# Optimization experiments

Measured on AMD Instinct MI355X. Metric: run time of the kernel, lower is better.

## Reference

```python
import jax, jax.numpy as jnp
import numpy as np

N = 8192
D = 128
LMBD = 0.1
SPARSITY = 0.99  # fraction of zero entries in A


def setup_inputs() -> dict:
    key = jax.random.key(0)
    kA, kW = jax.random.split(key)
    u = jax.random.uniform(kA, (N, N), dtype=jnp.float32)
    A = jnp.where(u > SPARSITY, u, 0.0)
    W = jax.random.normal(kW, (N, D), dtype=jnp.float32) * 0.02
    b = jnp.zeros((D,), dtype=jnp.float32)
    return {"A": A, "W": W, "b": b}


def reference(A, W, b):
    # model(tf.eye(N)) with Dense(d) == eye(N) @ W + b == W + b  -> [N, d]
    Y = W + b
    # main loss: 0.5 * sum(mask * (A - Y Y^T)^2), mask = (A > 0)
    R = A - jnp.matmul(Y, Y.T)  # [N, N]
    main_loss = 0.5 * jnp.sum(jnp.where(A > 0, R * R, 0.0))
    # reg loss: lmbd/2 * ||Y||_F^2
    reg_loss = 0.5 * LMBD * jnp.sum(Y * Y)
    return main_loss + reg_loss
```

## Files before the change

kernel.cpp:

```cpp
#include <hip/hip_runtime.h>

#define N 8192
#define D 128
#define MAXNZ 256

__device__ __forceinline__ float wave_reduce(float p) {
    #pragma unroll
    for (int off = 32; off > 0; off >>= 1)
        p += __shfl_xor(p, off, 64);
    return p;
}

__global__ __launch_bounds__(256, 8)
void gf_main_kernel(const float* __restrict__ A,
                    const float* __restrict__ W,
                    const float* __restrict__ b,
                    float* __restrict__ partials) {
    __shared__ int   s_col[4][MAXNZ];
    __shared__ float s_val[4][MAXNZ];
    __shared__ float s_bsum[4];

    const int lane = threadIdx.x & 63;
    const int w    = threadIdx.x >> 6;
    const int row  = blockIdx.x * 4 + w;

    const float2 bb = ((const float2*)b)[lane];
    float2 yi = ((const float2*)(W + (size_t)row * D))[lane];
    yi.x += bb.x; yi.y += bb.y;

    const float4* Arow = (const float4*)(A + (size_t)row * N);
    const unsigned long long ltmask = (lane == 63) ? ~0ull >> 1 : (1ull << lane) - 1ull;
    int cnt = 0;
    for (int it = 0; it < N / 256; ++it) {
        const float4 a4 = Arow[it * 64 + lane];
        const float av[4] = {a4.x, a4.y, a4.z, a4.w};
        #pragma unroll
        for (int q = 0; q < 4; ++q) {
            const unsigned long long m = __ballot(av[q] > 0.0f);
            if (av[q] > 0.0f) {
                const int pos = cnt + __popcll(m & ((1ull << lane) - 1ull));
                if (pos < MAXNZ) {
                    s_col[w][pos] = it * 256 + lane * 4 + q;
                    s_val[w][pos] = av[q];
                }
            }
            cnt += __popcll(m);
        }
    }
    if (cnt > MAXNZ) cnt = MAXNZ;
    __syncthreads();

    float acc = 0.0f;
    for (int t = 0; t < cnt; t += 4) {
        float p[4];
        float av[4];
        #pragma unroll
        for (int k = 0; k < 4; ++k) {
            const bool valid = (t + k) < cnt;
            const int  idx   = valid ? (t + k) : 0;
            const int  j     = s_col[w][idx];
            av[k]            = valid ? s_val[w][idx] : 0.0f;
            const float2 yj  = ((const float2*)(W + (size_t)j * D))[lane];
            p[k] = yi.x * (yj.x + bb.x) + yi.y * (yj.y + bb.y);
        }
        #pragma unroll
        for (int off = 32; off > 0; off >>= 1) {
            #pragma unroll
            for (int k = 0; k < 4; ++k)
                p[k] += __shfl_xor(p[k], off, 64);
        }
        #pragma unroll
        for (int k = 0; k < 4; ++k) {
            if ((t + k) < cnt) {
                const float r = av[k] - p[k];
                acc += r * r;
            }
        }
    }

    const float reg = wave_reduce(yi.x * yi.x + yi.y * yi.y);
    const float total = 0.5f * acc + 0.05f * reg;
    if (lane == 0) s_bsum[w] = total;
    __syncthreads();
    if (threadIdx.x == 0)
        partials[blockIdx.x] = s_bsum[0] + s_bsum[1] + s_bsum[2] + s_bsum[3];
}

__global__ __launch_bounds__(256)
void gf_reduce_kernel(const float* __restrict__ partials, float* __restrict__ out) {
    __shared__ float s_ws[4];
    const int lane = threadIdx.x & 63;
    const int w    = threadIdx.x >> 6;
    float s = 0.0f;
    for (int i = threadIdx.x; i < N / 4; i += 256) s += partials[i];
    s = wave_reduce(s);
    if (lane == 0) s_ws[w] = s;
    __syncthreads();
    if (threadIdx.x == 0) out[0] = s_ws[0] + s_ws[1] + s_ws[2] + s_ws[3];
}

extern "C" void kernel_launch(void* const* d_in, const int* in_sizes, int n_in,
                              void* d_out, int out_size, void* d_ws, size_t ws_size,
                              hipStream_t stream) {
    const float* A = (const float*)d_in[0];
    const float* W = (const float*)d_in[1];
    const float* b = (const float*)d_in[2];
    float* out = (float*)d_out;
    float* partials = (float*)d_ws;

    gf_main_kernel<<<dim3(N / 4), dim3(256), 0, stream>>>(A, W, b, partials);
    gf_reduce_kernel<<<dim3(1), dim3(256), 0, stream>>>(partials, out);
}
```

Measured before the change: 413.4 us.

## Software-pipeline A row loads and W gathers with register prefetch

The scan over each A row now keeps four float4 loads per lane in flight and prefetches the next 1024-column chunk while ballot-compacting the current one. The gather loop over nonzeros also prefetches the next group of four W rows before reducing the current group. Occupancy bounds drop from 8 to 6 blocks per CU to make room for the extra prefetch registers. The goal is more memory-level parallelism on the 256 MB A stream, at the cost of fewer resident waves.

After: 391.4 us. 1.06x faster.

```diff
diff --git a/kernel.cpp b/kernel.cpp
--- a/kernel.cpp
+++ b/kernel.cpp
@@ -11,7 +11,7 @@
     return p;
 }
 
-__global__ __launch_bounds__(256, 8)
+__global__ __launch_bounds__(256, 6)
 void gf_main_kernel(const float* __restrict__ A,
                     const float* __restrict__ W,
                     const float* __restrict__ b,
@@ -29,46 +29,84 @@
     yi.x += bb.x; yi.y += bb.y;
 
     const float4* Arow = (const float4*)(A + (size_t)row * N);
-    const unsigned long long ltmask = (lane == 63) ? ~0ull >> 1 : (1ull << lane) - 1ull;
+    const unsigned long long lmask = (1ull << lane) - 1ull;
+
+    float4 pf[4];
+    #pragma unroll
+    for (int k = 0; k < 4; ++k) pf[k] = Arow[k * 64 + lane];
+
     int cnt = 0;
-    for (int it = 0; it < N / 256; ++it) {
-        const float4 a4 = Arow[it * 64 + lane];
-        const float av[4] = {a4.x, a4.y, a4.z, a4.w};
+    for (int it = 0; it < 8; ++it) {
+        float4 cur[4];
         #pragma unroll
-        for (int q = 0; q < 4; ++q) {
-            const unsigned long long m = __ballot(av[q] > 0.0f);
-            if (av[q] > 0.0f) {
-                const int pos = cnt + __popcll(m & ((1ull << lane) - 1ull));
-                if (pos < MAXNZ) {
-                    s_col[w][pos] = it * 256 + lane * 4 + q;
-                    s_val[w][pos] = av[q];
+        for (int k = 0; k < 4; ++k) cur[k] = pf[k];
+        if (it < 7) {
+            #pragma unroll
+            for (int k = 0; k < 4; ++k)
+                pf[k] = Arow[(it + 1) * 256 + k * 64 + lane];
+        }
+        #pragma unroll
+        for (int k = 0; k < 4; ++k) {
+            const int base_col = (it * 4 + k) * 256 + lane * 4;
+            const float av4[4] = {cur[k].x, cur[k].y, cur[k].z, cur[k].w};
+            #pragma unroll
+            for (int q = 0; q < 4; ++q) {
+                const unsigned long long m = __ballot(av4[q] > 0.0f);
+                if (av4[q] > 0.0f) {
+                    const int pos = cnt + __popcll(m & lmask);
+                    if (pos < MAXNZ) {
+                        s_col[w][pos] = base_col + q;
+                        s_val[w][pos] = av4[q];
+                    }
                 }
+                cnt += __popcll(m);
             }
-            cnt += __popcll(m);
         }
     }
     if (cnt > MAXNZ) cnt = MAXNZ;
     __syncthreads();
 
     float acc = 0.0f;
+    float2 yjn[4];
+    float  avn[4];
+    #pragma unroll
+    for (int k = 0; k < 4; ++k) {
+        const bool valid = k < cnt;
+        const int  idx   = valid ? k : 0;
+        const int  j     = s_col[w][idx];
+        avn[k]           = valid ? s_val[w][idx] : 0.0f;
+        yjn[k]           = ((const float2*)(W + (size_t)j * D))[lane];
+    }
+
     for (int t = 0; t < cnt; t += 4) {
+        float2 yj[4];
+        float  av[4];
+        #pragma unroll
+        for (int k = 0; k < 4; ++k) { yj[k] = yjn[k]; av[k] = avn[k]; }
+
+        if (t + 4 < cnt) {
+            #pragma unroll
+            for (int k = 0; k < 4; ++k) {
+                const bool valid = (t + 4 + k) < cnt;
+                const int  idx   = valid ? (t + 4 + k) : 0;
+                const int  j     = s_col[w][idx];
+                avn[k]           = valid ? s_val[w][idx] : 0.0f;
+                yjn[k]           = ((const float2*)(W + (size_t)j * D))[lane];
+            }
+        }
+
         float p[4];
-        float av[4];
         #pragma unroll
-        for (int k = 0; k < 4; ++k) {
-            const bool valid = (t + k) < cnt;
-            const int  idx   = valid ? (t + k) : 0;
-            const int  j     = s_col[w][idx];
-            av[k]            = valid ? s_val[w][idx] : 0.0f;
-            const float2 yj  = ((const float2*)(W + (size_t)j * D))[lane];
-            p[k] = yi.x * (yj.x + bb.x) + yi.y * (yj.y + bb.y);
-        }
+        for (int k = 0; k < 4; ++k)
+            p[k] = yi.x * (yj[k].x + bb.x) + yi.y * (yj[k].y + bb.y);
+
         #pragma unroll
         for (int off = 32; off > 0; off >>= 1) {
             #pragma unroll
             for (int k = 0; k < 4; ++k)
                 p[k] += __shfl_xor(p[k], off, 64);
         }
+
         #pragma unroll
         for (int k = 0; k < 4; ++k) {
             if ((t + k) < cnt) {
```

## Replace sparse gather with dense fp16 MFMA tiled Y·Yᵀ and masked loss

Applied to the files above, without the earlier changes.

Replaces the per-row nonzero compaction and gather of Y rows with a dense 128x128-tile computation of Y·Yᵀ using fp16 MFMA 16x16x32 instructions. A prep kernel first converts Y=W+b to fp16 and computes the regularization term. The tile kernel then streams A once and accumulates masked squared residuals. This removes the ballot/compaction and the scattered row gathers but does full dense N²·D work. The fp16 inputs may lose precision relative to the fp32 reference.

Result: faster. 383.7 us (-7.2%).

```diff
diff --git a/kernel.cpp b/kernel.cpp
--- a/kernel.cpp
+++ b/kernel.cpp
@@ -1,8 +1,15 @@
 #include <hip/hip_runtime.h>
+#include <hip/hip_fp16.h>
 
 #define N 8192
 #define D 128
-#define MAXNZ 256
+
+typedef _Float16 f16x8 __attribute__((ext_vector_type(8)));
+typedef float    f32x4 __attribute__((ext_vector_type(4)));
+
+#define YH_OFF    0
+#define PART_OFF  (4u * 1024 * 1024)
+#define NPART     (4096 + 2048)
 
 __device__ __forceinline__ float wave_reduce(float p) {
     #pragma unroll
@@ -11,79 +18,94 @@
     return p;
 }
 
-__global__ __launch_bounds__(256, 8)
-void gf_main_kernel(const float* __restrict__ A,
-                    const float* __restrict__ W,
-                    const float* __restrict__ b,
-                    float* __restrict__ partials) {
-    __shared__ int   s_col[4][MAXNZ];
-    __shared__ float s_val[4][MAXNZ];
+__global__ __launch_bounds__(256)
+void gf_prep_kernel(const float* __restrict__ W, const float* __restrict__ b,
+                    __half* __restrict__ Yh, float* __restrict__ partials) {
     __shared__ float s_bsum[4];
-
     const int lane = threadIdx.x & 63;
     const int w    = threadIdx.x >> 6;
     const int row  = blockIdx.x * 4 + w;
 
     const float2 bb = ((const float2*)b)[lane];
-    float2 yi = ((const float2*)(W + (size_t)row * D))[lane];
-    yi.x += bb.x; yi.y += bb.y;
+    float2 y = ((const float2*)(W + (size_t)row * D))[lane];
+    y.x += bb.x; y.y += bb.y;
+    __half2 h;
+    h.x = __float2half_rn(y.x);
+    h.y = __float2half_rn(y.y);
+    ((__half2*)(Yh + (size_t)row * D))[lane] = h;
 
-    const float4* Arow = (const float4*)(A + (size_t)row * N);
-    const unsigned long long ltmask = (lane == 63) ? ~0ull >> 1 : (1ull << lane) - 1ull;
-    int cnt = 0;
-    for (int it = 0; it < N / 256; ++it) {
-        const float4 a4 = Arow[it * 64 + lane];
-        const float av[4] = {a4.x, a4.y, a4.z, a4.w};
+    const float reg = wave_reduce(y.x * y.x + y.y * y.y);
+    if (lane == 0) s_bsum[w] = reg;
+    __syncthreads();
+    if (threadIdx.x == 0)
+        partials[4096 + blockIdx.x] = 0.05f * (s_bsum[0] + s_bsum[1] + s_bsum[2] + s_bsum[3]);
+}
+
+__global__ __launch_bounds__(256)
+void gf_tile_kernel(const float* __restrict__ A,
+                    const __half* __restrict__ Yh,
+                    float* __restrict__ partials) {
+    __shared__ float s_bsum[4];
+    const int lane = threadIdx.x & 63;
+    const int w    = threadIdx.x >> 6;
+    const int tx   = blockIdx.x & 63;
+    const int ty   = blockIdx.x >> 6;
+    const int i0   = ty * 128 + (w >> 1) * 64;
+    const int j0   = tx * 128 + (w & 1) * 64;
+    const int lr   = lane & 15;
+    const int kg   = lane >> 4;
+
+    f32x4 acc[4][4];
+    #pragma unroll
+    for (int bi = 0; bi < 4; ++bi)
         #pragma unroll
-        for (int q = 0; q < 4; ++q) {
-            const unsigned long long m = __ballot(av[q] > 0.0f);
-            if (av[q] > 0.0f) {
-                const int pos = cnt + __popcll(m & ((1ull << lane) - 1ull));
-                if (pos < MAXNZ) {
-                    s_col[w][pos] = it * 256 + lane * 4 + q;
-                    s_val[w][pos] = av[q];
+        for (int bj = 0; bj < 4; ++bj)
+            acc[bi][bj] = (f32x4){0.f, 0.f, 0.f, 0.f};
+
+    #pragma unroll
+    for (int ks = 0; ks < 4; ++ks) {
+        f16x8 af[4], bf[4];
+        #pragma unroll
+        for (int t = 0; t < 4; ++t) {
+            af[t] = *(const f16x8*)(Yh + (size_t)(i0 + t * 16 + lr) * D + ks * 32 + kg * 8);
+            bf[t] = *(const f16x8*)(Yh + (size_t)(j0 + t * 16 + lr) * D + ks * 32 + kg * 8);
+        }
+        #pragma unroll
+        for (int bi = 0; bi < 4; ++bi)
+            #pragma unroll
+            for (int bj = 0; bj < 4; ++bj)
+                acc[bi][bj] = __builtin_amdgcn_mfma_f32_16x16x32_f16(
+                    af[bi], bf[bj], acc[bi][bj], 0, 0, 0);
+    }
+
+    float loss = 0.0f;
+    #pragma unroll
+    for (int bi = 0; bi < 4; ++bi) {
+        float a[4][4];
+        #pragma unroll
+        for (int r = 0; r < 4; ++r) {
+            const float* Ap = A + (size_t)(i0 + bi * 16 + kg * 4 + r) * N + j0 + lr;
+            #pragma unroll
+            for (int bj = 0; bj < 4; ++bj)
+                a[r][bj] = Ap[bj * 16];
+        }
+        #pragma unroll
+        for (int r = 0; r < 4; ++r)
+            #pragma unroll
+            for (int bj = 0; bj < 4; ++bj) {
+                const float av = a[r][bj];
+                if (av > 0.0f) {
+                    const float d = av - acc[bi][bj][r];
+                    loss += d * d;
                 }
             }
-            cnt += __popcll(m);
-        }
-    }
-    if (cnt > MAXNZ) cnt = MAXNZ;
-    __syncthreads();
-
-    float acc = 0.0f;
-    for (int t = 0; t < cnt; t += 4) {
-        float p[4];
-        float av[4];
-        #pragma unroll
-        for (int k = 0; k < 4; ++k) {
-            const bool valid = (t + k) < cnt;
-            const int  idx   = valid ? (t + k) : 0;
-            const int  j     = s_col[w][idx];
-            av[k]            = valid ? s_val[w][idx] : 0.0f;
-            const float2 yj  = ((const float2*)(W + (size_t)j * D))[lane];
-            p[k] = yi.x * (yj.x + bb.x) + yi.y * (yj.y + bb.y);
-        }
-        #pragma unroll
-        for (int off = 32; off > 0; off >>= 1) {
-            #pragma unroll
-            for (int k = 0; k < 4; ++k)
-                p[k] += __shfl_xor(p[k], off, 64);
-        }
-        #pragma unroll
-        for (int k = 0; k < 4; ++k) {
-            if ((t + k) < cnt) {
-                const float r = av[k] - p[k];
-                acc += r * r;
-            }
-        }
     }
 
-    const float reg = wave_reduce(yi.x * yi.x + yi.y * yi.y);
-    const float total = 0.5f * acc + 0.05f * reg;
-    if (lane == 0) s_bsum[w] = total;
+    loss = wave_reduce(loss);
+    if (lane == 0) s_bsum[w] = loss;
     __syncthreads();
     if (threadIdx.x == 0)
-        partials[blockIdx.x] = s_bsum[0] + s_bsum[1] + s_bsum[2] + s_bsum[3];
+        partials[blockIdx.x] = 0.5f * (s_bsum[0] + s_bsum[1] + s_bsum[2] + s_bsum[3]);
 }
 
 __global__ __launch_bounds__(256)
@@ -92,7 +114,7 @@
     const int lane = threadIdx.x & 63;
     const int w    = threadIdx.x >> 6;
     float s = 0.0f;
-    for (int i = threadIdx.x; i < N / 4; i += 256) s += partials[i];
+    for (int i = threadIdx.x; i < NPART; i += 256) s += partials[i];
     s = wave_reduce(s);
     if (lane == 0) s_ws[w] = s;
     __syncthreads();
@@ -106,8 +128,12 @@
     const float* W = (const float*)d_in[1];
     const float* b = (const float*)d_in[2];
     float* out = (float*)d_out;
-    float* partials = (float*)d_ws;
 
-    gf_main_kernel<<<dim3(N / 4), dim3(256), 0, stream>>>(A, W, b, partials);
+    char*   ws       = (char*)d_ws;
+    __half* Yh       = (__half*)(ws + YH_OFF);
+    float*  partials = (float*)(ws + PART_OFF);
+
+    gf_prep_kernel<<<dim3(N / 4), dim3(256), 0, stream>>>(W, b, Yh, partials);
+    gf_tile_kernel<<<dim3(4096), dim3(256), 0, stream>>>(A, Yh, partials);
     gf_reduce_kernel<<<dim3(1), dim3(256), 0, stream>>>(partials, out);
 }
```
